# Optimization experiments

Hardware: AMD Instinct MI355X
Metric: run time of the kernel (lower is better)

The kernel has to match this reference:

```python
import jax, jax.numpy as jnp
import numpy as np


def _cdist(a, b):
    # Euclidean pairwise distances, [N, M]
    d2 = (jnp.sum(a * a, axis=1)[:, None]
          + jnp.sum(b * b, axis=1)[None, :]
          - 2.0 * (a @ b.T))
    return jnp.sqrt(jnp.maximum(d2, 0.0))


def setup_inputs() -> dict:
    key = jax.random.key(0)
    k1, k2 = jax.random.split(key)
    N, M, D = 12288, 12288, 3
    true_pos = jax.random.normal(k1, (N, D), dtype=jnp.float32)
    pred_pos = jax.random.normal(k2, (M, D), dtype=jnp.float32)
    return {"true_pos": true_pos, "pred_pos": pred_pos}


def reference(true_pos, pred_pos):
    dists = _cdist(true_pos.astype(jnp.float32), pred_pos.astype(jnp.float32))
    mins = jnp.min(dists, axis=1)        # per true point -> nearest pred
    mins_seeds = jnp.min(dists, axis=0)  # per pred point -> nearest true
    loss = jnp.mean(mins)
    loss_seeds = jnp.mean(mins_seeds)
    just_in_case_losses = (loss, loss_seeds)
    # use_loss=True branch
    return (loss + loss_seeds, mins_seeds, just_in_case_losses)
```

## Files before the change

kernel.cpp:

```cpp
#include <hip/hip_runtime.h>
#include <cfloat>

typedef __bf16 bf16x8 __attribute__((ext_vector_type(8)));
typedef unsigned short ushort8 __attribute__((ext_vector_type(8)));
typedef float f32x16 __attribute__((ext_vector_type(16)));

#define S_SLICES 4

static __device__ __forceinline__ unsigned short f2bf(float x) {
    unsigned u = __float_as_uint(x);
    return (unsigned short)((u + 0x7FFFu + ((u >> 16) & 1u)) >> 16);
}
static __device__ __forceinline__ float bfbits2f(unsigned short h) {
    return __uint_as_float(((unsigned)h) << 16);
}

__global__ __launch_bounds__(256) void prep_kernel(
    const float* __restrict__ A, const float* __restrict__ B,
    ushort8* __restrict__ RFA, ushort8* __restrict__ CFA,
    ushort8* __restrict__ RFB, ushort8* __restrict__ CFB,
    float* __restrict__ hdr, int n, int m, int RTn, int RTm)
{
    const int i = blockIdx.x * 256 + threadIdx.x;
    if (i < 8) hdr[i] = 0.f;
    const unsigned short one = 0x3F80;

#pragma unroll
    for (int side = 0; side < 2; ++side) {
        const int cntPts = side ? RTm * 32 : RTn * 32;
        if (i >= cntPts) continue;
        const float* P = side ? B : A;
        const int lim = side ? m : n;
        ushort8* RF = side ? RFB : RFA;
        ushort8* CF = side ? CFB : CFA;

        float x = 0.f, y = 0.f, z = 0.f, nrm = 1e30f;
        if (i < lim) { x = P[3*i]; y = P[3*i+1]; z = P[3*i+2];
                       nrm = fmaf(x, x, fmaf(y, y, z * z)); }
        const unsigned short hx = f2bf(x), hy = f2bf(y), hz = f2bf(z);
        const unsigned short lx = f2bf(x - bfbits2f(hx)),
                             ly = f2bf(y - bfbits2f(hy)),
                             lz = f2bf(z - bfbits2f(hz));
        const unsigned short nhx = f2bf(-2.f * bfbits2f(hx)),
                             nhy = f2bf(-2.f * bfbits2f(hy)),
                             nhz = f2bf(-2.f * bfbits2f(hz));
        const unsigned short nlx = f2bf(-2.f * bfbits2f(lx)),
                             nly = f2bf(-2.f * bfbits2f(ly)),
                             nlz = f2bf(-2.f * bfbits2f(lz));
        float r = nrm;
        const unsigned short s1 = f2bf(r); r -= bfbits2f(s1);
        const unsigned short s2 = f2bf(r); r -= bfbits2f(s2);
        const unsigned short s3 = f2bf(r);

        const int t = i >> 5, l5 = i & 31;
        ushort8 rq0 = { nhx, nhy, nhz, nhx, nhy, nhz, nlx, nly };
        ushort8 rq1 = { nlz, s1, s2, s3, one, one, one, 0 };
        RF[t * 64 + l5]      = rq0;
        RF[t * 64 + 32 + l5] = rq1;
        ushort8 cq0 = { hx, hy, hz, lx, ly, lz, hx, hy };
        ushort8 cq1 = { hz, one, one, one, s1, s2, s3, 0 };
        CF[t * 64 + l5]      = cq0;
        CF[t * 64 + 32 + l5] = cq1;
    }
}

#define MINC(C)                                             \
    _Pragma("unroll")                                       \
    for (int r = 0; r < 16; ++r) macc[r] = fminf(macc[r], (C)[r]);

__global__ __launch_bounds__(256, 4) void pairmin_kernel(
    const bf16x8* __restrict__ RFA, const bf16x8* __restrict__ CFA,
    const bf16x8* __restrict__ RFB, const bf16x8* __restrict__ CFB,
    float* __restrict__ sbuf, int RTn, int RTm)
{
    const int lane = threadIdx.x & 63;
    const int wave = threadIdx.x >> 6;

    const bf16x8* RF; const bf16x8* CF; float* sb; int rtCount, ctCount, stride;
    if (blockIdx.z == 0) { RF = RFA; CF = CFB; rtCount = RTn; ctCount = RTm;
                           sb = sbuf; stride = RTn * 32; }
    else                 { RF = RFB; CF = CFA; rtCount = RTm; ctCount = RTn;
                           sb = sbuf + (size_t)S_SLICES * RTn * 32;
                           stride = RTm * 32; }

    const int rt = blockIdx.x * 4 + wave;
    if (rt >= rtCount) return;
    sb += (size_t)blockIdx.y * stride;

    const int ctPer = (ctCount + S_SLICES - 1) / S_SLICES;
    const int ctBeg = min(blockIdx.y * ctPer, ctCount);
    const int ctEnd = min(ctBeg + ctPer, ctCount);

    const bf16x8 afrag = RF[rt * 64 + lane];
    const f32x16 zc = {};

    float macc[16];
#pragma unroll
    for (int r = 0; r < 16; ++r) macc[r] = FLT_MAX;

    if (ctBeg < ctEnd) {
        int ct = ctBeg;
        const int last = ctEnd - 1;
        bf16x8 q0 = CF[(size_t)ct * 64 + lane];
        bf16x8 q1 = CF[(size_t)min(ct + 1, last) * 64 + lane];
        bf16x8 q2 = CF[(size_t)min(ct + 2, last) * 64 + lane];
        bf16x8 q3 = CF[(size_t)min(ct + 3, last) * 64 + lane];
        f32x16 C0 = __builtin_amdgcn_mfma_f32_32x32x16_bf16(afrag, q0, zc, 0, 0, 0);
        f32x16 C1 = __builtin_amdgcn_mfma_f32_32x32x16_bf16(afrag, q1, zc, 0, 0, 0);

        for (; ct + 7 < ctEnd; ct += 4) {
            q0 = CF[(size_t)(ct + 4) * 64 + lane];
            MINC(C0);
            C0 = __builtin_amdgcn_mfma_f32_32x32x16_bf16(afrag, q2, zc, 0, 0, 0);
            q1 = CF[(size_t)(ct + 5) * 64 + lane];
            MINC(C1);
            C1 = __builtin_amdgcn_mfma_f32_32x32x16_bf16(afrag, q3, zc, 0, 0, 0);
            q2 = CF[(size_t)(ct + 6) * 64 + lane];
            MINC(C0);
            C0 = __builtin_amdgcn_mfma_f32_32x32x16_bf16(afrag, q0, zc, 0, 0, 0);
            q3 = CF[(size_t)(ct + 7) * 64 + lane];
            MINC(C1);
            C1 = __builtin_amdgcn_mfma_f32_32x32x16_bf16(afrag, q1, zc, 0, 0, 0);
        }
        MINC(C0);
        MINC(C1);
        if (ct + 2 < ctEnd) {
            const f32x16 C =
                __builtin_amdgcn_mfma_f32_32x32x16_bf16(afrag, q2, zc, 0, 0, 0);
            MINC(C);
        }
        if (ct + 3 < ctEnd) {
            const f32x16 C =
                __builtin_amdgcn_mfma_f32_32x32x16_bf16(afrag, q3, zc, 0, 0, 0);
            MINC(C);
        }
        for (int t = ct + 4; t < ctEnd; ++t) {
            const bf16x8 b = CF[(size_t)t * 64 + lane];
            const f32x16 C =
                __builtin_amdgcn_mfma_f32_32x32x16_bf16(afrag, b, zc, 0, 0, 0);
            MINC(C);
        }
    }

#pragma unroll
    for (int r = 0; r < 16; ++r) {
        float v = macc[r];
        v = fminf(v, __shfl_xor(v, 1, 64));
        v = fminf(v, __shfl_xor(v, 2, 64));
        v = fminf(v, __shfl_xor(v, 4, 64));
        v = fminf(v, __shfl_xor(v, 8, 64));
        v = fminf(v, __shfl_xor(v, 16, 64));
        macc[r] = v;
    }
    if ((lane & 31) == 0) {
        const int q4 = (lane >> 5) * 4;
        float* dst = sb + rt * 32;
#pragma unroll
        for (int r = 0; r < 16; ++r)
            dst[(r & 3) + 8 * (r >> 2) + q4] = macc[r];
    }
}

__global__ __launch_bounds__(256) void finalize_kernel(
    const float* __restrict__ sbuf, float* __restrict__ hdr,
    float* __restrict__ out, int n, int m, int RTn, int RTm)
{
    const int i = blockIdx.x * 256 + threadIdx.x;
    const int strideA = RTn * 32, strideB = RTm * 32;
    const float* sbB = sbuf + (size_t)S_SLICES * strideA;

    float sa = 0.f, sb_ = 0.f;
    if (i < n) {
        float s = FLT_MAX;
#pragma unroll
        for (int k = 0; k < S_SLICES; ++k) s = fminf(s, sbuf[(size_t)k * strideA + i]);
        sa = sqrtf(fmaxf(s, 0.f));
    }
    if (i < m) {
        float s = FLT_MAX;
#pragma unroll
        for (int k = 0; k < S_SLICES; ++k) s = fminf(s, sbB[(size_t)k * strideB + i]);
        const float v = sqrtf(fmaxf(s, 0.f));
        out[1 + i] = v;
        sb_ = v;
    }

#pragma unroll
    for (int off = 32; off > 0; off >>= 1) {
        sa  += __shfl_down(sa,  off, 64);
        sb_ += __shfl_down(sb_, off, 64);
    }
    __shared__ float reda[4], redb[4];
    const int wave = threadIdx.x >> 6;
    const int lane = threadIdx.x & 63;
    if (lane == 0) { reda[wave] = sa; redb[wave] = sb_; }
    __syncthreads();

    if (threadIdx.x == 0) {
        const float ta = reda[0] + reda[1] + reda[2] + reda[3];
        const float tb = redb[0] + redb[1] + redb[2] + redb[3];
        atomicAdd(&hdr[0], ta);
        atomicAdd(&hdr[1], tb);
        __threadfence();
        const unsigned ticket = atomicAdd((unsigned*)&hdr[2], 1u);
        if (ticket == (unsigned)(gridDim.x - 1)) {
            const float fa = atomicAdd(&hdr[0], 0.f);
            const float fb = atomicAdd(&hdr[1], 0.f);
            const float loss = fa / (float)n;
            const float loss_seeds = fb / (float)m;
            out[0] = loss + loss_seeds;
            out[1 + m] = loss;
            out[2 + m] = loss_seeds;
        }
    }
}

extern "C" void kernel_launch(void* const* d_in, const int* in_sizes, int n_in,
                              void* d_out, int out_size, void* d_ws, size_t ws_size,
                              hipStream_t stream) {
    const int n = in_sizes[0] / 3;
    const int m = in_sizes[1] / 3;
    const float* A = (const float*)d_in[0];
    const float* B = (const float*)d_in[1];
    float* out = (float*)d_out;

    const int RTn = (n + 31) / 32, RTm = (m + 31) / 32;
    char* p = (char*)d_ws;
    float*   hdr  = (float*)p;    p += 64;
    float*   sbuf = (float*)p;    p += (size_t)S_SLICES * (RTn + RTm) * 32 * 4;
    ushort8* RFA  = (ushort8*)p;  p += (size_t)RTn * 64 * 16;
    ushort8* CFA  = (ushort8*)p;  p += (size_t)RTn * 64 * 16;
    ushort8* RFB  = (ushort8*)p;  p += (size_t)RTm * 64 * 16;
    ushort8* CFB  = (ushort8*)p;

    const int maxPts = ((RTn > RTm) ? RTn : RTm) * 32;
    prep_kernel<<<(maxPts + 255) / 256, 256, 0, stream>>>(
        A, B, RFA, CFA, RFB, CFB, hdr, n, m, RTn, RTm);

    const int maxRT = (RTn > RTm) ? RTn : RTm;
    dim3 grid((maxRT + 3) / 4, S_SLICES, 2);
    pairmin_kernel<<<grid, 256, 0, stream>>>(
        (const bf16x8*)RFA, (const bf16x8*)CFA,
        (const bf16x8*)RFB, (const bf16x8*)CFB, sbuf, RTn, RTm);

    const int maxnm = (n > m) ? n : m;
    finalize_kernel<<<(maxnm + 255) / 256, 256, 0, stream>>>(
        sbuf, hdr, out, n, m, RTn, RTm);
}
```

Measured before the change: 78.16 us.

## Compute distance matrix once and derive both row and column minima

Before, the pairwise distance tiles were computed twice, once for each direction's minima. Now each tile is computed once: row minima are kept in registers, and column minima are reduced per tile, combined across the block's waves through shared memory, and written as per-block candidates. The finalize kernel then reduces these candidates across row-blocks. This halves the MFMA work but adds shared-memory traffic, extra block barriers, a large colcand buffer (GX x m floats) and a longer final reduction, with occupancy lowered from 4 to 3 blocks.

```diff
diff --git a/kernel.cpp b/kernel.cpp
--- a/kernel.cpp
+++ b/kernel.cpp
@@ -5,7 +5,8 @@
 typedef unsigned short ushort8 __attribute__((ext_vector_type(8)));
 typedef float f32x16 __attribute__((ext_vector_type(16)));
 
-#define S_SLICES 4
+#define CT_SLICES 8
+#define CHUNK 48
 
 static __device__ __forceinline__ unsigned short f2bf(float x) {
     unsigned u = __float_as_uint(x);
@@ -17,8 +18,7 @@
 
 __global__ __launch_bounds__(256) void prep_kernel(
     const float* __restrict__ A, const float* __restrict__ B,
-    ushort8* __restrict__ RFA, ushort8* __restrict__ CFA,
-    ushort8* __restrict__ RFB, ushort8* __restrict__ CFB,
+    ushort8* __restrict__ RFA, ushort8* __restrict__ CFB,
     float* __restrict__ hdr, int n, int m, int RTn, int RTm)
 {
     const int i = blockIdx.x * 256 + threadIdx.x;
@@ -31,8 +31,6 @@
         if (i >= cntPts) continue;
         const float* P = side ? B : A;
         const int lim = side ? m : n;
-        ushort8* RF = side ? RFB : RFA;
-        ushort8* CF = side ? CFB : CFA;
 
         float x = 0.f, y = 0.f, z = 0.f, nrm = 1e30f;
         if (i < lim) { x = P[3*i]; y = P[3*i+1]; z = P[3*i+2];
@@ -41,26 +39,29 @@
         const unsigned short lx = f2bf(x - bfbits2f(hx)),
                              ly = f2bf(y - bfbits2f(hy)),
                              lz = f2bf(z - bfbits2f(hz));
-        const unsigned short nhx = f2bf(-2.f * bfbits2f(hx)),
-                             nhy = f2bf(-2.f * bfbits2f(hy)),
-                             nhz = f2bf(-2.f * bfbits2f(hz));
-        const unsigned short nlx = f2bf(-2.f * bfbits2f(lx)),
-                             nly = f2bf(-2.f * bfbits2f(ly)),
-                             nlz = f2bf(-2.f * bfbits2f(lz));
         float r = nrm;
         const unsigned short s1 = f2bf(r); r -= bfbits2f(s1);
         const unsigned short s2 = f2bf(r); r -= bfbits2f(s2);
         const unsigned short s3 = f2bf(r);
 
         const int t = i >> 5, l5 = i & 31;
-        ushort8 rq0 = { nhx, nhy, nhz, nhx, nhy, nhz, nlx, nly };
-        ushort8 rq1 = { nlz, s1, s2, s3, one, one, one, 0 };
-        RF[t * 64 + l5]      = rq0;
-        RF[t * 64 + 32 + l5] = rq1;
-        ushort8 cq0 = { hx, hy, hz, lx, ly, lz, hx, hy };
-        ushort8 cq1 = { hz, one, one, one, s1, s2, s3, 0 };
-        CF[t * 64 + l5]      = cq0;
-        CF[t * 64 + 32 + l5] = cq1;
+        if (side == 0) {
+            const unsigned short nhx = f2bf(-2.f * bfbits2f(hx)),
+                                 nhy = f2bf(-2.f * bfbits2f(hy)),
+                                 nhz = f2bf(-2.f * bfbits2f(hz));
+            const unsigned short nlx = f2bf(-2.f * bfbits2f(lx)),
+                                 nly = f2bf(-2.f * bfbits2f(ly)),
+                                 nlz = f2bf(-2.f * bfbits2f(lz));
+            ushort8 rq0 = { nhx, nhy, nhz, nhx, nhy, nhz, nlx, nly };
+            ushort8 rq1 = { nlz, s1, s2, s3, one, one, one, 0 };
+            RFA[t * 64 + l5]      = rq0;
+            RFA[t * 64 + 32 + l5] = rq1;
+        } else {
+            ushort8 cq0 = { hx, hy, hz, lx, ly, lz, hx, hy };
+            ushort8 cq1 = { hz, one, one, one, s1, s2, s3, 0 };
+            CFB[t * 64 + l5]      = cq0;
+            CFB[t * 64 + 32 + l5] = cq1;
+        }
     }
 }
 
@@ -68,78 +69,111 @@
     _Pragma("unroll")                                       \
     for (int r = 0; r < 16; ++r) macc[r] = fminf(macc[r], (C)[r]);
 
-__global__ __launch_bounds__(256, 4) void pairmin_kernel(
-    const bf16x8* __restrict__ RFA, const bf16x8* __restrict__ CFA,
-    const bf16x8* __restrict__ RFB, const bf16x8* __restrict__ CFB,
-    float* __restrict__ sbuf, int RTn, int RTm)
+static __device__ __forceinline__ float tree16(const f32x16& C) {
+    const float a0 = fminf(fminf(C[0],  C[1]),  C[2]);
+    const float a1 = fminf(fminf(C[3],  C[4]),  C[5]);
+    const float a2 = fminf(fminf(C[6],  C[7]),  C[8]);
+    const float a3 = fminf(fminf(C[9],  C[10]), C[11]);
+    const float a4 = fminf(fminf(C[12], C[13]), C[14]);
+    return fminf(fminf(fminf(a0, a1), a2), fminf(fminf(a3, a4), C[15]));
+}
+
+#define RETIRE(C, ttr) do {                                 \
+    MINC(C);                                                \
+    lcol[abase + (ttr) * 32 + l5] = tree16(C);              \
+} while (0)
+
+__global__ __launch_bounds__(256, 3) void pairmin_kernel(
+    const bf16x8* __restrict__ RFA, const bf16x8* __restrict__ CFB,
+    float* __restrict__ sbuf, float* __restrict__ colcand,
+    int RTn, int RTm)
 {
     const int lane = threadIdx.x & 63;
     const int wave = threadIdx.x >> 6;
-
-    const bf16x8* RF; const bf16x8* CF; float* sb; int rtCount, ctCount, stride;
-    if (blockIdx.z == 0) { RF = RFA; CF = CFB; rtCount = RTn; ctCount = RTm;
-                           sb = sbuf; stride = RTn * 32; }
-    else                 { RF = RFB; CF = CFA; rtCount = RTm; ctCount = RTn;
-                           sb = sbuf + (size_t)S_SLICES * RTn * 32;
-                           stride = RTm * 32; }
+    const int l5 = lane & 31;
 
     const int rt = blockIdx.x * 4 + wave;
-    if (rt >= rtCount) return;
-    sb += (size_t)blockIdx.y * stride;
-
-    const int ctPer = (ctCount + S_SLICES - 1) / S_SLICES;
-    const int ctBeg = min(blockIdx.y * ctPer, ctCount);
-    const int ctEnd = min(ctBeg + ctPer, ctCount);
-
-    const bf16x8 afrag = RF[rt * 64 + lane];
+    const bool live = rt < RTn;
+    const int rtc = live ? rt : RTn - 1;
+    const int strideA = RTn * 32, strideB = RTm * 32;
+
+    const int ctPer = (RTm + CT_SLICES - 1) / CT_SLICES;
+    const int ctBeg = min((int)blockIdx.y * ctPer, RTm);
+    const int ctEnd = min(ctBeg + ctPer, RTm);
+
+    const bf16x8 afrag = RFA[rtc * 64 + lane];
     const f32x16 zc = {};
 
+    __shared__ float lcol[8 * CHUNK * 32];
+    const int abase = (wave * 2 + (lane >> 5)) * (CHUNK * 32);
+
     float macc[16];
 #pragma unroll
     for (int r = 0; r < 16; ++r) macc[r] = FLT_MAX;
 
-    if (ctBeg < ctEnd) {
-        int ct = ctBeg;
-        const int last = ctEnd - 1;
-        bf16x8 q0 = CF[(size_t)ct * 64 + lane];
-        bf16x8 q1 = CF[(size_t)min(ct + 1, last) * 64 + lane];
-        bf16x8 q2 = CF[(size_t)min(ct + 2, last) * 64 + lane];
-        bf16x8 q3 = CF[(size_t)min(ct + 3, last) * 64 + lane];
-        f32x16 C0 = __builtin_amdgcn_mfma_f32_32x32x16_bf16(afrag, q0, zc, 0, 0, 0);
-        f32x16 C1 = __builtin_amdgcn_mfma_f32_32x32x16_bf16(afrag, q1, zc, 0, 0, 0);
-
-        for (; ct + 7 < ctEnd; ct += 4) {
-            q0 = CF[(size_t)(ct + 4) * 64 + lane];
-            MINC(C0);
-            C0 = __builtin_amdgcn_mfma_f32_32x32x16_bf16(afrag, q2, zc, 0, 0, 0);
-            q1 = CF[(size_t)(ct + 5) * 64 + lane];
-            MINC(C1);
-            C1 = __builtin_amdgcn_mfma_f32_32x32x16_bf16(afrag, q3, zc, 0, 0, 0);
-            q2 = CF[(size_t)(ct + 6) * 64 + lane];
-            MINC(C0);
-            C0 = __builtin_amdgcn_mfma_f32_32x32x16_bf16(afrag, q0, zc, 0, 0, 0);
-            q3 = CF[(size_t)(ct + 7) * 64 + lane];
-            MINC(C1);
-            C1 = __builtin_amdgcn_mfma_f32_32x32x16_bf16(afrag, q1, zc, 0, 0, 0);
-        }
-        MINC(C0);
-        MINC(C1);
-        if (ct + 2 < ctEnd) {
-            const f32x16 C =
-                __builtin_amdgcn_mfma_f32_32x32x16_bf16(afrag, q2, zc, 0, 0, 0);
-            MINC(C);
-        }
-        if (ct + 3 < ctEnd) {
-            const f32x16 C =
-                __builtin_amdgcn_mfma_f32_32x32x16_bf16(afrag, q3, zc, 0, 0, 0);
-            MINC(C);
-        }
-        for (int t = ct + 4; t < ctEnd; ++t) {
-            const bf16x8 b = CF[(size_t)t * 64 + lane];
-            const f32x16 C =
-                __builtin_amdgcn_mfma_f32_32x32x16_bf16(afrag, b, zc, 0, 0, 0);
-            MINC(C);
-        }
+    for (int cb = ctBeg; cb < ctEnd; cb += CHUNK) {
+        const int T = min(CHUNK, ctEnd - cb);
+        const bf16x8* P = CFB + (size_t)cb * 64;
+
+        if (T >= 4) {
+            bf16x8 q0 = P[0 * 64 + lane];
+            bf16x8 q1 = P[1 * 64 + lane];
+            bf16x8 q2 = P[2 * 64 + lane];
+            bf16x8 q3 = P[3 * 64 + lane];
+            f32x16 C0 = __builtin_amdgcn_mfma_f32_32x32x16_bf16(afrag, q0, zc, 0, 0, 0);
+            f32x16 C1 = __builtin_amdgcn_mfma_f32_32x32x16_bf16(afrag, q1, zc, 0, 0, 0);
+
+            int t = 0;
+            for (; t + 7 < T; t += 4) {
+                q0 = P[(size_t)(t + 4) * 64 + lane];
+                RETIRE(C0, t);
+                C0 = __builtin_amdgcn_mfma_f32_32x32x16_bf16(afrag, q2, zc, 0, 0, 0);
+                q1 = P[(size_t)(t + 5) * 64 + lane];
+                RETIRE(C1, t + 1);
+                C1 = __builtin_amdgcn_mfma_f32_32x32x16_bf16(afrag, q3, zc, 0, 0, 0);
+                q2 = P[(size_t)(t + 6) * 64 + lane];
+                RETIRE(C0, t + 2);
+                C0 = __builtin_amdgcn_mfma_f32_32x32x16_bf16(afrag, q0, zc, 0, 0, 0);
+                q3 = P[(size_t)(t + 7) * 64 + lane];
+                RETIRE(C1, t + 3);
+                C1 = __builtin_amdgcn_mfma_f32_32x32x16_bf16(afrag, q1, zc, 0, 0, 0);
+            }
+            RETIRE(C0, t);
+            RETIRE(C1, t + 1);
+            if (t + 2 < T) {
+                const f32x16 C =
+                    __builtin_amdgcn_mfma_f32_32x32x16_bf16(afrag, q2, zc, 0, 0, 0);
+                RETIRE(C, t + 2);
+            }
+            if (t + 3 < T) {
+                const f32x16 C =
+                    __builtin_amdgcn_mfma_f32_32x32x16_bf16(afrag, q3, zc, 0, 0, 0);
+                RETIRE(C, t + 3);
+            }
+            for (int u = t + 4; u < T; ++u) {
+                const bf16x8 b = P[(size_t)u * 64 + lane];
+                const f32x16 C =
+                    __builtin_amdgcn_mfma_f32_32x32x16_bf16(afrag, b, zc, 0, 0, 0);
+                RETIRE(C, u);
+            }
+        } else {
+            for (int u = 0; u < T; ++u) {
+                const bf16x8 b = P[(size_t)u * 64 + lane];
+                const f32x16 C =
+                    __builtin_amdgcn_mfma_f32_32x32x16_bf16(afrag, b, zc, 0, 0, 0);
+                RETIRE(C, u);
+            }
+        }
+
+        __syncthreads();
+        for (int idx = threadIdx.x; idx < T * 32; idx += 256) {
+            float v = lcol[idx];
+#pragma unroll
+            for (int a = 1; a < 8; ++a)
+                v = fminf(v, lcol[a * (CHUNK * 32) + idx]);
+            colcand[(size_t)blockIdx.x * strideB + (size_t)cb * 32 + idx] = v;
+        }
+        __syncthreads();
     }
 
 #pragma unroll
@@ -152,9 +186,9 @@
         v = fminf(v, __shfl_xor(v, 16, 64));
         macc[r] = v;
     }
-    if ((lane & 31) == 0) {
+    if (live && l5 == 0) {
         const int q4 = (lane >> 5) * 4;
-        float* dst = sb + rt * 32;
+        float* dst = sbuf + (size_t)blockIdx.y * strideA + rt * 32;
 #pragma unroll
         for (int r = 0; r < 16; ++r)
             dst[(r & 3) + 8 * (r >> 2) + q4] = macc[r];
@@ -162,24 +196,26 @@
 }
 
 __global__ __launch_bounds__(256) void finalize_kernel(
-    const float* __restrict__ sbuf, float* __restrict__ hdr,
-    float* __restrict__ out, int n, int m, int RTn, int RTm)
+    const float* __restrict__ sbuf, const float* __restrict__ colcand,
+    float* __restrict__ hdr, float* __restrict__ out,
+    int n, int m, int RTn, int RTm, int GX)
 {
     const int i = blockIdx.x * 256 + threadIdx.x;
     const int strideA = RTn * 32, strideB = RTm * 32;
-    const float* sbB = sbuf + (size_t)S_SLICES * strideA;
 
     float sa = 0.f, sb_ = 0.f;
     if (i < n) {
         float s = FLT_MAX;
 #pragma unroll
-        for (int k = 0; k < S_SLICES; ++k) s = fminf(s, sbuf[(size_t)k * strideA + i]);
+        for (int k = 0; k < CT_SLICES; ++k)
+            s = fminf(s, sbuf[(size_t)k * strideA + i]);
         sa = sqrtf(fmaxf(s, 0.f));
     }
     if (i < m) {
         float s = FLT_MAX;
-#pragma unroll
-        for (int k = 0; k < S_SLICES; ++k) s = fminf(s, sbB[(size_t)k * strideB + i]);
+#pragma unroll 4
+        for (int g = 0; g < GX; ++g)
+            s = fminf(s, colcand[(size_t)g * strideB + i]);
         const float v = sqrtf(fmaxf(s, 0.f));
         out[1 + i] = v;
         sb_ = v;
@@ -225,25 +261,24 @@
     float* out = (float*)d_out;
 
     const int RTn = (n + 31) / 32, RTm = (m + 31) / 32;
+    const int GX = (RTn + 3) / 4;
     char* p = (char*)d_ws;
-    float*   hdr  = (float*)p;    p += 64;
-    float*   sbuf = (float*)p;    p += (size_t)S_SLICES * (RTn + RTm) * 32 * 4;
-    ushort8* RFA  = (ushort8*)p;  p += (size_t)RTn * 64 * 16;
-    ushort8* CFA  = (ushort8*)p;  p += (size_t)RTn * 64 * 16;
-    ushort8* RFB  = (ushort8*)p;  p += (size_t)RTm * 64 * 16;
-    ushort8* CFB  = (ushort8*)p;
-
-    const int maxPts = ((RTn > RTm) ? RTn : RTm) * 32;
+    float*   hdr     = (float*)p;   p += 64;
+    float*   sbuf    = (float*)p;   p += (size_t)CT_SLICES * RTn * 32 * 4;
+    float*   colcand = (float*)p;   p += (size_t)GX * RTm * 32 * 4;
+    ushort8* RFA     = (ushort8*)p; p += (size_t)RTn * 64 * 16;
+    ushort8* CFB     = (ushort8*)p;
+
+    const int maxRT = (RTn > RTm) ? RTn : RTm;
+    const int maxPts = maxRT * 32;
     prep_kernel<<<(maxPts + 255) / 256, 256, 0, stream>>>(
-        A, B, RFA, CFA, RFB, CFB, hdr, n, m, RTn, RTm);
-
-    const int maxRT = (RTn > RTm) ? RTn : RTm;
-    dim3 grid((maxRT + 3) / 4, S_SLICES, 2);
+        A, B, RFA, CFB, hdr, n, m, RTn, RTm);
+
+    dim3 grid(GX, CT_SLICES, 1);
     pairmin_kernel<<<grid, 256, 0, stream>>>(
-        (const bf16x8*)RFA, (const bf16x8*)CFA,
-        (const bf16x8*)RFB, (const bf16x8*)CFB, sbuf, RTn, RTm);
+        (const bf16x8*)RFA, (const bf16x8*)CFB, sbuf, colcand, RTn, RTm);
 
     const int maxnm = (n > m) ? n : m;
     finalize_kernel<<<(maxnm + 255) / 256, 256, 0, stream>>>(
-        sbuf, hdr, out, n, m, RTn, RTm);
-}
+        sbuf, colcand, hdr, out, n, m, RTn, RTm, GX);
+}
```

Measured after the change: 92.42 us. 1.18x slower.
